# Kernel tuning notes

Hardware: AMD Instinct MI355X
Metric: run time of the kernel (lower is better)

The kernel has to match this reference:

```python
import jax, jax.numpy as jnp
import numpy as np

B, H, S, F_RANK, D_HEAD = 1, 8, 4096, 64, 64
NEG = -1e9


def setup_inputs() -> dict:
    key = jax.random.key(0)
    k1, k2, k3, k4 = jax.random.split(key, 4)
    v = jax.random.normal(k1, (B, H, S, D_HEAD), dtype=jnp.float32)
    A1 = jax.random.normal(k2, (B, H, S, F_RANK), dtype=jnp.float32)
    A2 = jax.random.normal(k3, (B, H, F_RANK, S), dtype=jnp.float32)
    mask = jax.random.randint(k4, (B, 1, S, S), 0, 2, dtype=jnp.int32)
    return {"v": v, "A1": A1, "A2": A2, "mask": mask, "len_q": S}


def reference(v, A1, A2, mask, len_q):
    # Rank-f factorized scores: [B,H,len_q,len_q]
    scores = jnp.einsum('bhsf,bhft->bhst', A1[:, :, :len_q, :], A2[:, :, :, :len_q])
    scores = scores[:mask.shape[0]]
    # masked_fill(mask != 0, -1e9)
    scores = jnp.where(mask[:, :, :len_q, :len_q] != 0, jnp.float32(NEG), scores)
    attn = jax.nn.softmax(scores, axis=-1)  # dropout is identity in eval mode
    output = jnp.einsum('bhst,bhtd->bhsd', attn, v[:, :, :len_q, :])
    return (output, attn)
```

## Files before the change

### kernel.cpp

```cpp
#include <hip/hip_runtime.h>
#include <hip/hip_bf16.h>
#include <stdint.h>

#define S_LEN 4096
#define NHEAD 8
#define L2E   1.44269504088896340736f

typedef __attribute__((ext_vector_type(8))) short bf16x8;
typedef __attribute__((ext_vector_type(4))) float f32x4;
typedef unsigned short u16;
typedef unsigned int   u32;

#define MFMA16(a,b,c) __builtin_amdgcn_mfma_f32_16x16x32_bf16((a),(b),(c),0,0,0)
#define EXP2F(x) __builtin_amdgcn_exp2f((x))

__device__ __forceinline__ void gl_lds16(const void* g, void* l) {
  __builtin_amdgcn_global_load_lds((const __attribute__((address_space(1))) void*)g,
                                   (__attribute__((address_space(3))) void*)l, 16, 0, 0);
}

__device__ __forceinline__ short f2bf(float x) {
  __hip_bfloat16 h = __float2bfloat16(x);
  return *(short*)&h;
}

#define WS_A1HI 0u
#define WS_A1LO (4u<<20)
#define WS_A2HI (8u<<20)
#define WS_A2LO (12u<<20)
#define WS_VHI  (16u<<20)
#define WS_VLO  (20u<<20)
#define WS_BM   (24u<<20)
#define WS_INVL (26u<<20)

__global__ void pk_mask(const int* __restrict__ mask, u32* __restrict__ bmT) {
  const int sb = blockIdx.x >> 4;
  const int t  = (blockIdx.x & 15) * 256 + threadIdx.x;
  u32 w = 0;
  #pragma unroll
  for (int j = 0; j < 32; ++j)
    w |= (mask[(size_t)(sb * 32 + j) * S_LEN + t] != 0 ? 1u : 0u) << j;
  bmT[sb * S_LEN + t] = w;
}

__global__ void pk_split(const float* __restrict__ src, u16* __restrict__ hi, u16* __restrict__ lo) {
  const int i = blockIdx.x * 256 + threadIdx.x;
  float4 x = ((const float4*)src)[i];
  ushort4 hv, lv;
  #pragma unroll
  for (int j = 0; j < 4; ++j) {
    float xv = ((const float*)&x)[j];
    __hip_bfloat16 hb = __float2bfloat16(xv);
    float hf = __bfloat162float(hb);
    __hip_bfloat16 lb = __float2bfloat16(xv - hf);
    ((u16*)&hv)[j] = *(u16*)&hb;
    ((u16*)&lv)[j] = *(u16*)&lb;
  }
  ((ushort4*)hi)[i] = hv;
  ((ushort4*)lo)[i] = lv;
}

__global__ void pk_tsplit(const float* __restrict__ src, u16* __restrict__ hi, u16* __restrict__ lo,
                          int chunk_stride, int row_stride) {
  const int h = blockIdx.x >> 6, ci = blockIdx.x & 63;
  const float* base = src + (size_t)h * (S_LEN * 64) + (size_t)ci * chunk_stride;
  __shared__ float tile[64][65];
  const int jr = threadIdx.x & 63, ir = threadIdx.x >> 6;
  #pragma unroll
  for (int p = 0; p < 16; ++p) {
    int i = p * 4 + ir;
    tile[i][jr] = base[(size_t)i * row_stride + jr];
  }
  __syncthreads();
  const size_t ob = (size_t)(h * 64 + ci) * 4096;
  #pragma unroll
  for (int p = 0; p < 16; ++p) {
    int o = p * 256 + threadIdx.x;
    int r = o >> 6;
    int cc = (o & 63) ^ ((r & 7) << 3);
    float xv = tile[cc][r];
    __hip_bfloat16 hb = __float2bfloat16(xv);
    float hf = __bfloat162float(hb);
    __hip_bfloat16 lb = __float2bfloat16(xv - hf);
    hi[ob + o] = *(u16*)&hb;
    lo[ob + o] = *(u16*)&lb;
  }
}

__launch_bounds__(512, 2)
__global__ void fattn_pass1(const u16* __restrict__ a1hi, const u16* __restrict__ a1lo,
                            const u16* __restrict__ a2hi, const u16* __restrict__ a2lo,
                            const u32* __restrict__ bmT,  float* __restrict__ invl) {
  const int h   = blockIdx.x & 7;
  const int sb  = blockIdx.x >> 3;
  const int tid = threadIdx.x;
  const int w = tid >> 6, lane = tid & 63;
  const int g = lane >> 4, c = lane & 15;
  const int wsr = w >> 1;
  const int wth = w & 1;
  const int sbase = sb * 128 + wsr * 32;
  const int sb32  = sb * 4 + wsr;

  __shared__ __align__(16) char smem[33792];
  float* mll = (float*)(smem + 32768);

  bf16x8 a1f[2][2][2];
  #pragma unroll
  for (int mt = 0; mt < 2; ++mt)
    #pragma unroll
    for (int kk = 0; kk < 2; ++kk) {
      size_t base = (size_t)(h * S_LEN + sbase + mt * 16 + c) * 64 + kk * 32 + g * 8;
      a1f[mt][kk][0] = *(const bf16x8*)(a1hi + base);
      a1f[mt][kk][1] = *(const bf16x8*)(a1lo + base);
    }

  float rl[2][4];
  #pragma unroll
  for (int mt = 0; mt < 2; ++mt)
    #pragma unroll
    for (int r = 0; r < 4; ++r) rl[mt][r] = 0.f;

  const u32* bmrow = bmT + (size_t)sb32 * S_LEN;

  auto stage2 = [&](int bufi, int ci) {
    const size_t tb = (size_t)(h * 64 + ci) * 4096;
    char* lb = smem + bufi * 16384;
    const int off = w * 1024 + lane * 16;
    gl_lds16((const char*)(a2hi + tb) + off, lb +        w * 1024);
    gl_lds16((const char*)(a2lo + tb) + off, lb + 8192 + w * 1024);
  };

  stage2(0, 0);
  __syncthreads();

  #pragma unroll 1
  for (int ci = 0; ci < 64; ++ci) {
    if (ci < 63) stage2((ci + 1) & 1, ci + 1);

    const u16* base = (const u16*)(smem + (ci & 1) * 16384);

    f32x4 acc[2][2];
    #pragma unroll
    for (int mt = 0; mt < 2; ++mt)
      #pragma unroll
      for (int nt = 0; nt < 2; ++nt) acc[mt][nt] = (f32x4){0.f, 0.f, 0.f, 0.f};
    #pragma unroll
    for (int kk = 0; kk < 2; ++kk)
      #pragma unroll
      for (int nt = 0; nt < 2; ++nt) {
        int eb = (wth * 32 + nt * 16 + c) * 64 + ((kk * 32 + g * 8) ^ ((c & 7) << 3));
        bf16x8 bh = *(const bf16x8*)(base + eb);
        bf16x8 bl = *(const bf16x8*)(base + 4096 + eb);
        #pragma unroll
        for (int mt = 0; mt < 2; ++mt) {
          acc[mt][nt] = MFMA16(a1f[mt][kk][0], bh, acc[mt][nt]);
          acc[mt][nt] = MFMA16(a1f[mt][kk][0], bl, acc[mt][nt]);
          acc[mt][nt] = MFMA16(a1f[mt][kk][1], bh, acc[mt][nt]);
        }
      }

    const u32 mw0 = bmrow[ci * 64 + wth * 32 + c];
    const u32 mw1 = bmrow[ci * 64 + wth * 32 + 16 + c];
    #pragma unroll
    for (int mt = 0; mt < 2; ++mt)
      #pragma unroll
      for (int nt = 0; nt < 2; ++nt) {
        const u32 mwv = nt ? mw1 : mw0;
        #pragma unroll
        for (int r = 0; r < 4; ++r) {
          float ex = EXP2F(acc[mt][nt][r] * L2E);
          rl[mt][r] += ((mwv >> (mt * 16 + g * 4 + r)) & 1u) ? 0.f : ex;
        }
      }

    __syncthreads();
  }

  #pragma unroll
  for (int mt = 0; mt < 2; ++mt)
    #pragma unroll
    for (int r = 0; r < 4; ++r) {
      float s = rl[mt][r];
      #pragma unroll
      for (int off = 1; off < 16; off <<= 1) s += __shfl_xor(s, off);
      rl[mt][r] = s;
    }
  __syncthreads();
  if (c == 0) {
    #pragma unroll
    for (int mt = 0; mt < 2; ++mt)
      #pragma unroll
      for (int r = 0; r < 4; ++r)
        mll[w * 32 + mt * 16 + g * 4 + r] = rl[mt][r];
  }
  __syncthreads();
  if (wth == 0 && c == 0) {
    #pragma unroll
    for (int mt = 0; mt < 2; ++mt)
      #pragma unroll
      for (int r = 0; r < 4; ++r) {
        float tot = rl[mt][r] + mll[(w ^ 1) * 32 + mt * 16 + g * 4 + r];
        invl[h * S_LEN + sbase + mt * 16 + g * 4 + r] = 1.0f / tot;
      }
  }
}

__launch_bounds__(512, 2)
__global__ void fattn_pass2(const u16* __restrict__ a1hi, const u16* __restrict__ a1lo,
                            const u16* __restrict__ a2hi, const u16* __restrict__ a2lo,
                            const u16* __restrict__ vhi,  const u16* __restrict__ vlo,
                            const u32* __restrict__ bmT,  const float* __restrict__ invl,
                            float* __restrict__ dout) {
  const int h   = blockIdx.x & 7;
  const int sb  = blockIdx.x >> 3;
  const int tid = threadIdx.x;
  const int w = tid >> 6, lane = tid & 63;
  const int g = lane >> 4, c = lane & 15;
  const int wsr = w >> 1;
  const int wth = w & 1;
  const int sbase = sb * 128 + wsr * 32;
  const int sb32  = sb * 4 + wsr;

  __shared__ __align__(16) char smem[103424];
  float* atbf = (float*)(smem + 65536);
  float* mll  = (float*)(smem + 102400);
  (void)mll;

  bf16x8 a1f[2][2][2];
  #pragma unroll
  for (int mt = 0; mt < 2; ++mt)
    #pragma unroll
    for (int kk = 0; kk < 2; ++kk) {
      size_t base = (size_t)(h * S_LEN + sbase + mt * 16 + c) * 64 + kk * 32 + g * 8;
      a1f[mt][kk][0] = *(const bf16x8*)(a1hi + base);
      a1f[mt][kk][1] = *(const bf16x8*)(a1lo + base);
    }

  float inv[2][4];
  #pragma unroll
  for (int mt = 0; mt < 2; ++mt)
    #pragma unroll
    for (int r = 0; r < 4; ++r)
      inv[mt][r] = invl[h * S_LEN + sbase + mt * 16 + g * 4 + r];

  f32x4 oacc[2][4];
  #pragma unroll
  for (int mt = 0; mt < 2; ++mt)
    #pragma unroll
    for (int dt = 0; dt < 4; ++dt) oacc[mt][dt] = (f32x4){0.f, 0.f, 0.f, 0.f};

  const u32* bmrow = bmT + (size_t)sb32 * S_LEN;
  float* aout = dout + (size_t)NHEAD * S_LEN * 64;
  float* myatb = atbf + w * 1152;

  auto stage_all = [&](int bufi, int ci) {
    const size_t tb = (size_t)(h * 64 + ci) * 4096;
    char* lb = smem + bufi * 32768;
    const int off = w * 1024 + lane * 16;
    gl_lds16((const char*)(a2hi + tb) + off, lb +         w * 1024);
    gl_lds16((const char*)(a2lo + tb) + off, lb +  8192 + w * 1024);
    gl_lds16((const char*)(vhi  + tb) + off, lb + 16384 + w * 1024);
    gl_lds16((const char*)(vlo  + tb) + off, lb + 24576 + w * 1024);
  };

  stage_all(0, 0);
  __syncthreads();

  #pragma unroll 1
  for (int ci = 0; ci < 64; ++ci) {
    if (ci < 63) stage_all((ci + 1) & 1, ci + 1);

    const u16* base = (const u16*)(smem + (ci & 1) * 32768);

    f32x4 acc[2][2];
    #pragma unroll
    for (int mt = 0; mt < 2; ++mt)
      #pragma unroll
      for (int nt = 0; nt < 2; ++nt) acc[mt][nt] = (f32x4){0.f, 0.f, 0.f, 0.f};
    #pragma unroll
    for (int kk = 0; kk < 2; ++kk)
      #pragma unroll
      for (int nt = 0; nt < 2; ++nt) {
        int eb = (wth * 32 + nt * 16 + c) * 64 + ((kk * 32 + g * 8) ^ ((c & 7) << 3));
        bf16x8 bh = *(const bf16x8*)(base + eb);
        bf16x8 bl = *(const bf16x8*)(base + 4096 + eb);
        #pragma unroll
        for (int mt = 0; mt < 2; ++mt) {
          acc[mt][nt] = MFMA16(a1f[mt][kk][0], bh, acc[mt][nt]);
          acc[mt][nt] = MFMA16(a1f[mt][kk][0], bl, acc[mt][nt]);
          acc[mt][nt] = MFMA16(a1f[mt][kk][1], bh, acc[mt][nt]);
        }
      }

    const u32 mw0 = bmrow[ci * 64 + wth * 32 + c];
    const u32 mw1 = bmrow[ci * 64 + wth * 32 + 16 + c];
    #pragma unroll
    for (int mt = 0; mt < 2; ++mt)
      #pragma unroll
      for (int nt = 0; nt < 2; ++nt) {
        const u32 mwv = nt ? mw1 : mw0;
        #pragma unroll
        for (int r = 0; r < 4; ++r) {
          float ex = EXP2F(acc[mt][nt][r] * L2E);
          float av = ((mwv >> (mt * 16 + g * 4 + r)) & 1u) ? 0.f : ex * inv[mt][r];
          myatb[(mt * 16 + g * 4 + r) * 36 + nt * 16 + c] = av;
        }
      }

    asm volatile("" ::: "memory");

    bf16x8 af[2];
    #pragma unroll
    for (int mt = 0; mt < 2; ++mt) {
      const float* arow = myatb + (mt * 16 + c) * 36 + g * 8;
      float4 f0 = *(const float4*)(arow);
      float4 f1 = *(const float4*)(arow + 4);
      af[mt][0] = f2bf(f0.x); af[mt][1] = f2bf(f0.y);
      af[mt][2] = f2bf(f0.z); af[mt][3] = f2bf(f0.w);
      af[mt][4] = f2bf(f1.x); af[mt][5] = f2bf(f1.y);
      af[mt][6] = f2bf(f1.z); af[mt][7] = f2bf(f1.w);
    }

    {
      const size_t rb = (size_t)(h * S_LEN + sbase) * S_LEN + ci * 64 + wth * 32;
      #pragma unroll
      for (int i = 0; i < 8; ++i) {
        float2 vv = *(const float2*)(myatb + (i * 4 + g) * 36 + 2 * c);
        *(float2*)(aout + rb + (size_t)(i * 4 + g) * S_LEN + 2 * c) = vv;
      }
    }

    #pragma unroll
    for (int dt = 0; dt < 4; ++dt) {
      int ve = (dt * 16 + c) * 64 + ((wth * 32 + g * 8) ^ ((c & 7) << 3));
      bf16x8 bvh = *(const bf16x8*)(base + 8192 + ve);
      bf16x8 bvl = *(const bf16x8*)(base + 12288 + ve);
      #pragma unroll
      for (int mt = 0; mt < 2; ++mt) {
        oacc[mt][dt] = MFMA16(af[mt], bvh, oacc[mt][dt]);
        oacc[mt][dt] = MFMA16(af[mt], bvl, oacc[mt][dt]);
      }
    }

    __syncthreads();
  }

  __syncthreads();
  float* outx = (float*)smem;
  if (wth == 1) {
    #pragma unroll
    for (int mt = 0; mt < 2; ++mt)
      #pragma unroll
      for (int dt = 0; dt < 4; ++dt)
        #pragma unroll
        for (int r = 0; r < 4; ++r)
          outx[wsr * 2112 + (mt * 16 + g * 4 + r) * 66 + dt * 16 + c] = oacc[mt][dt][r];
  }
  __syncthreads();
  if (wth == 0) {
    #pragma unroll
    for (int mt = 0; mt < 2; ++mt)
      #pragma unroll
      for (int dt = 0; dt < 4; ++dt)
        #pragma unroll
        for (int r = 0; r < 4; ++r) {
          float vv = oacc[mt][dt][r] + outx[wsr * 2112 + (mt * 16 + g * 4 + r) * 66 + dt * 16 + c];
          int s = sbase + mt * 16 + g * 4 + r;
          dout[(size_t)(h * S_LEN + s) * 64 + dt * 16 + c] = vv;
        }
  }
}

extern "C" void kernel_launch(void* const* d_in, const int* in_sizes, int n_in,
                              void* d_out, int out_size, void* d_ws, size_t ws_size,
                              hipStream_t stream) {
  (void)in_sizes; (void)n_in; (void)out_size; (void)ws_size;
  const float* v    = (const float*)d_in[0];
  const float* A1   = (const float*)d_in[1];
  const float* A2   = (const float*)d_in[2];
  const int*   mask = (const int*)d_in[3];
  float* out = (float*)d_out;
  char* ws = (char*)d_ws;

  u16* a1hi = (u16*)(ws + WS_A1HI);
  u16* a1lo = (u16*)(ws + WS_A1LO);
  u16* a2hi = (u16*)(ws + WS_A2HI);
  u16* a2lo = (u16*)(ws + WS_A2LO);
  u16* vhi  = (u16*)(ws + WS_VHI);
  u16* vlo  = (u16*)(ws + WS_VLO);
  u32* bmT  = (u32*)(ws + WS_BM);
  float* invl = (float*)(ws + WS_INVL);

  pk_mask  <<<2048, 256, 0, stream>>>(mask, bmT);
  pk_split <<<2048, 256, 0, stream>>>(A1, a1hi, a1lo);
  pk_tsplit<<<512,  256, 0, stream>>>(A2, a2hi, a2lo, 64, 4096);
  pk_tsplit<<<512,  256, 0, stream>>>(v,  vhi,  vlo,  4096, 64);
  fattn_pass1<<<256, 512, 0, stream>>>(a1hi, a1lo, a2hi, a2lo, bmT, invl);
  fattn_pass2<<<256, 512, 0, stream>>>(a1hi, a1lo, a2hi, a2lo, vhi, vlo, bmT, invl, out);
}
```

Baseline: 794.3 us.

## Halve block size to 4 waves, stage bf16 attention tile, store probs from registers

Both attention passes now run 256-thread blocks covering 64 query rows, with twice as many blocks, and each wave issues two async LDS loads per buffer instead of one. In pass 2, probabilities are kept in registers, converted to bf16 before being written to a smaller padded LDS tile, read back directly as MFMA operands, and written to the attention output straight from registers. This shrinks LDS per block, which should let more blocks fit per CU and removes the float LDS round trip. The trade-off is that the A2/V tiles are loaded twice as often in total, and the attention output stores are now scalar and less coalesced.

```diff
diff --git a/kernel.cpp b/kernel.cpp
--- a/kernel.cpp
+++ b/kernel.cpp
@@ -87,7 +87,7 @@
   }
 }
 
-__launch_bounds__(512, 2)
+__launch_bounds__(256, 2)
 __global__ void fattn_pass1(const u16* __restrict__ a1hi, const u16* __restrict__ a1lo,
                             const u16* __restrict__ a2hi, const u16* __restrict__ a2lo,
                             const u32* __restrict__ bmT,  float* __restrict__ invl) {
@@ -98,10 +98,10 @@
   const int g = lane >> 4, c = lane & 15;
   const int wsr = w >> 1;
   const int wth = w & 1;
-  const int sbase = sb * 128 + wsr * 32;
-  const int sb32  = sb * 4 + wsr;
-
-  __shared__ __align__(16) char smem[33792];
+  const int sbase = sb * 64 + wsr * 32;
+  const int sb32  = sb * 2 + wsr;
+
+  __shared__ __align__(16) char smem[33280];
   float* mll = (float*)(smem + 32768);
 
   bf16x8 a1f[2][2][2];
@@ -125,9 +125,12 @@
   auto stage2 = [&](int bufi, int ci) {
     const size_t tb = (size_t)(h * 64 + ci) * 4096;
     char* lb = smem + bufi * 16384;
-    const int off = w * 1024 + lane * 16;
-    gl_lds16((const char*)(a2hi + tb) + off, lb +        w * 1024);
-    gl_lds16((const char*)(a2lo + tb) + off, lb + 8192 + w * 1024);
+    #pragma unroll
+    for (int i = 0; i < 2; ++i) {
+      const int off = w * 2048 + i * 1024 + lane * 16;
+      gl_lds16((const char*)(a2hi + tb) + off, lb +        off);
+      gl_lds16((const char*)(a2lo + tb) + off, lb + 8192 + off);
+    }
   };
 
   stage2(0, 0);
@@ -205,7 +208,7 @@
   }
 }
 
-__launch_bounds__(512, 2)
+__launch_bounds__(256, 2)
 __global__ void fattn_pass2(const u16* __restrict__ a1hi, const u16* __restrict__ a1lo,
                             const u16* __restrict__ a2hi, const u16* __restrict__ a2lo,
                             const u16* __restrict__ vhi,  const u16* __restrict__ vlo,
@@ -218,13 +221,11 @@
   const int g = lane >> 4, c = lane & 15;
   const int wsr = w >> 1;
   const int wth = w & 1;
-  const int sbase = sb * 128 + wsr * 32;
-  const int sb32  = sb * 4 + wsr;
-
-  __shared__ __align__(16) char smem[103424];
-  float* atbf = (float*)(smem + 65536);
-  float* mll  = (float*)(smem + 102400);
-  (void)mll;
+  const int sbase = sb * 64 + wsr * 32;
+  const int sb32  = sb * 2 + wsr;
+
+  __shared__ __align__(16) char smem[75776];
+  u16* atb = (u16*)(smem + 65536);
 
   bf16x8 a1f[2][2][2];
   #pragma unroll
@@ -251,16 +252,19 @@
 
   const u32* bmrow = bmT + (size_t)sb32 * S_LEN;
   float* aout = dout + (size_t)NHEAD * S_LEN * 64;
-  float* myatb = atbf + w * 1152;
+  u16* myatb = atb + w * 1280;
 
   auto stage_all = [&](int bufi, int ci) {
     const size_t tb = (size_t)(h * 64 + ci) * 4096;
     char* lb = smem + bufi * 32768;
-    const int off = w * 1024 + lane * 16;
-    gl_lds16((const char*)(a2hi + tb) + off, lb +         w * 1024);
-    gl_lds16((const char*)(a2lo + tb) + off, lb +  8192 + w * 1024);
-    gl_lds16((const char*)(vhi  + tb) + off, lb + 16384 + w * 1024);
-    gl_lds16((const char*)(vlo  + tb) + off, lb + 24576 + w * 1024);
+    #pragma unroll
+    for (int i = 0; i < 2; ++i) {
+      const int off = w * 2048 + i * 1024 + lane * 16;
+      gl_lds16((const char*)(a2hi + tb) + off, lb +         off);
+      gl_lds16((const char*)(a2lo + tb) + off, lb +  8192 + off);
+      gl_lds16((const char*)(vhi  + tb) + off, lb + 16384 + off);
+      gl_lds16((const char*)(vlo  + tb) + off, lb + 24576 + off);
+    }
   };
 
   stage_all(0, 0);
@@ -294,6 +298,7 @@
 
     const u32 mw0 = bmrow[ci * 64 + wth * 32 + c];
     const u32 mw1 = bmrow[ci * 64 + wth * 32 + 16 + c];
+    float av[2][2][4];
     #pragma unroll
     for (int mt = 0; mt < 2; ++mt)
       #pragma unroll
@@ -302,32 +307,34 @@
         #pragma unroll
         for (int r = 0; r < 4; ++r) {
           float ex = EXP2F(acc[mt][nt][r] * L2E);
-          float av = ((mwv >> (mt * 16 + g * 4 + r)) & 1u) ? 0.f : ex * inv[mt][r];
-          myatb[(mt * 16 + g * 4 + r) * 36 + nt * 16 + c] = av;
+          av[mt][nt][r] = ((mwv >> (mt * 16 + g * 4 + r)) & 1u) ? 0.f : ex * inv[mt][r];
         }
       }
 
+    #pragma unroll
+    for (int mt = 0; mt < 2; ++mt)
+      #pragma unroll
+      for (int nt = 0; nt < 2; ++nt)
+        #pragma unroll
+        for (int r = 0; r < 4; ++r)
+          myatb[(mt * 16 + g * 4 + r) * 40 + nt * 16 + c] = (u16)f2bf(av[mt][nt][r]);
+
     asm volatile("" ::: "memory");
 
     bf16x8 af[2];
     #pragma unroll
-    for (int mt = 0; mt < 2; ++mt) {
-      const float* arow = myatb + (mt * 16 + c) * 36 + g * 8;
-      float4 f0 = *(const float4*)(arow);
-      float4 f1 = *(const float4*)(arow + 4);
-      af[mt][0] = f2bf(f0.x); af[mt][1] = f2bf(f0.y);
-      af[mt][2] = f2bf(f0.z); af[mt][3] = f2bf(f0.w);
-      af[mt][4] = f2bf(f1.x); af[mt][5] = f2bf(f1.y);
-      af[mt][6] = f2bf(f1.z); af[mt][7] = f2bf(f1.w);
-    }
+    for (int mt = 0; mt < 2; ++mt)
+      af[mt] = *(const bf16x8*)(myatb + (mt * 16 + c) * 40 + g * 8);
 
     {
       const size_t rb = (size_t)(h * S_LEN + sbase) * S_LEN + ci * 64 + wth * 32;
       #pragma unroll
-      for (int i = 0; i < 8; ++i) {
-        float2 vv = *(const float2*)(myatb + (i * 4 + g) * 36 + 2 * c);
-        *(float2*)(aout + rb + (size_t)(i * 4 + g) * S_LEN + 2 * c) = vv;
-      }
+      for (int mt = 0; mt < 2; ++mt)
+        #pragma unroll
+        for (int nt = 0; nt < 2; ++nt)
+          #pragma unroll
+          for (int r = 0; r < 4; ++r)
+            aout[rb + (size_t)(mt * 16 + g * 4 + r) * S_LEN + nt * 16 + c] = av[mt][nt][r];
     }
 
     #pragma unroll
@@ -395,6 +402,6 @@
   pk_split <<<2048, 256, 0, stream>>>(A1, a1hi, a1lo);
   pk_tsplit<<<512,  256, 0, stream>>>(A2, a2hi, a2lo, 64, 4096);
   pk_tsplit<<<512,  256, 0, stream>>>(v,  vhi,  vlo,  4096, 64);
-  fattn_pass1<<<256, 512, 0, stream>>>(a1hi, a1lo, a2hi, a2lo, bmT, invl);
-  fattn_pass2<<<256, 512, 0, stream>>>(a1hi, a1lo, a2hi, a2lo, vhi, vlo, bmT, invl, out);
-}
+  fattn_pass1<<<512, 256, 0, stream>>>(a1hi, a1lo, a2hi, a2lo, bmT, invl);
+  fattn_pass2<<<512, 256, 0, stream>>>(a1hi, a1lo, a2hi, a2lo, vhi, vlo, bmT, invl, out);
+}
```

New measurement: 768.6 us. -3.2%, faster.
